# Kernel tuning notes

Hardware: AMD Instinct MI355X
Metric: run time of the kernel (lower is better)

Reference implementation:

```python
import jax, jax.numpy as jnp
import numpy as np

FP8_MAX = 448.0  # float8_e4m3fn max
NUM_HEADS = 16

def _fp8_quant_dequant(t):
    # per-(batch, head) symmetric scaling into fp8 e4m3 range, cast to fp8 and back
    amax = jnp.max(jnp.abs(t), axis=(-2, -1), keepdims=True)
    scale = FP8_MAX / jnp.maximum(amax, 1e-12)
    t8 = (t * scale).astype(jnp.float8_e4m3fn).astype(t.dtype)
    return t8 / scale

def setup_inputs() -> dict:
    key = jax.random.key(0)
    k1, k2, k3 = jax.random.split(key, 3)
    B, N, C = 2, 2048, 1024
    x = jax.random.normal(k1, (B, N, C), dtype=jnp.float32)
    w_qkv = jax.random.normal(k2, (C, 3 * C), dtype=jnp.float32) * (C ** -0.5)
    w_proj = jax.random.normal(k3, (C, C), dtype=jnp.float32) * (C ** -0.5)
    b_proj = jnp.zeros((C,), dtype=jnp.float32)
    return {"x": x, "w_qkv": w_qkv, "w_proj": w_proj, "b_proj": b_proj}

def reference(x, w_qkv, w_proj, b_proj):
    B, N, C = x.shape
    H = NUM_HEADS
    D = C // H
    scale = D ** -0.5
    qkv = (x @ w_qkv).reshape(B, N, 3, H, D).transpose(2, 0, 3, 1, 4)  # [3,B,H,N,D]
    q, k, v = qkv[0], qkv[1], qkv[2]
    # sage-style fp8 quantize/dequant of q and k fused into score computation
    q = _fp8_quant_dequant(q)
    k = _fp8_quant_dequant(k)
    scores = jnp.einsum('bhqd,bhkd->bhqk', q, k) * scale  # [B,H,N,N]
    causal = jnp.tril(jnp.ones((N, N), dtype=bool))
    scores = jnp.where(causal[None, None], scores, jnp.finfo(scores.dtype).min)
    attn = jax.nn.softmax(scores, axis=-1)
    out = jnp.einsum('bhqk,bhkd->bhqd', attn, v)  # [B,H,N,D]
    out = out.transpose(0, 2, 1, 3).reshape(B, N, C)
    return out @ w_proj + b_proj
```

## Files before the change

kernel.cpp:

```cpp
#include <hip/hip_runtime.h>

#define B_   2
#define N_   2048
#define C_   1024
#define H_   16
#define D_   64
#define BH_  (B_*H_)
#define NDH  (N_*D_)
#define M1   (B_*N_)

typedef __attribute__((ext_vector_type(4))) float    f32x4;
typedef __attribute__((ext_vector_type(8))) _Float16 f16x8;
typedef __attribute__((ext_vector_type(4))) _Float16 f16x4;

#define GLOAD_LDS(gp, lp) \
  __builtin_amdgcn_global_load_lds((const __attribute__((address_space(1))) void*)(gp), \
                                   (__attribute__((address_space(3))) void*)(lp), 16, 0, 0)

__global__ void k_cvt16(const float* __restrict__ in, _Float16* __restrict__ out, int n4) {
  int i = blockIdx.x * blockDim.x + threadIdx.x;
  if (i >= n4) return;
  float4 v = ((const float4*)in)[i];
  f16x4 o;
  o.x = (_Float16)v.x; o.y = (_Float16)v.y; o.z = (_Float16)v.z; o.w = (_Float16)v.w;
  ((f16x4*)out)[i] = o;
}

__global__ __launch_bounds__(256) void k_transmerge(const float* __restrict__ wq,
                                                    const float* __restrict__ wp,
                                                    _Float16* __restrict__ whT,
                                                    _Float16* __restrict__ wpT,
                                                    unsigned* __restrict__ amax_u) {
  if (blockIdx.x == 0 && threadIdx.x < 64) amax_u[threadIdx.x] = 0u;
  __shared__ _Float16 t[64][68];
  int idx = blockIdx.x;
  const float* in; _Float16* out; int Cc, cx, cy;
  if (idx < 768) { in = wq; out = whT; Cc = 3072; cx = idx % 48; cy = idx / 48; }
  else { idx -= 768; in = wp; out = wpT; Cc = 1024; cx = idx % 16; cy = idx / 16; }
  const int R = 1024;
  int c0 = cx * 64, r0 = cy * 64;
  int tid = threadIdx.x;
  int cq = tid & 15, rq = tid >> 4;
#pragma unroll
  for (int i = 0; i < 4; ++i) {
    int r = rq + i * 16;
    float4 v = *(const float4*)(in + (size_t)(r0 + r) * Cc + c0 + cq * 4);
    t[r][cq*4+0] = (_Float16)v.x;
    t[r][cq*4+1] = (_Float16)v.y;
    t[r][cq*4+2] = (_Float16)v.z;
    t[r][cq*4+3] = (_Float16)v.w;
  }
  __syncthreads();
#pragma unroll
  for (int i = 0; i < 4; ++i) {
    int c = rq + i * 16;
    f16x4 o;
    o.x = t[cq*4+0][c];
    o.y = t[cq*4+1][c];
    o.z = t[cq*4+2][c];
    o.w = t[cq*4+3][c];
    *(f16x4*)(out + (size_t)(c0 + c) * R + r0 + cq * 4) = o;
  }
}

__global__ __launch_bounds__(256) void k_gemm_qkv(const _Float16* __restrict__ A,
                                                  const _Float16* __restrict__ BT,
                                                  _Float16* __restrict__ qh,
                                                  _Float16* __restrict__ kh,
                                                  _Float16* __restrict__ vh,
                                                  unsigned* __restrict__ amax_u) {
  __shared__ __align__(16) _Float16 As[128 * 32];
  __shared__ __align__(16) _Float16 Bs[128 * 32];
  const int tid = threadIdx.x, lane = tid & 63, wave = tid >> 6;
  const int wm = wave >> 1, wn = wave & 1;
  const int mcol = lane & 15, quad = lane >> 4;
  const int m0 = blockIdx.x * 128, n0 = blockIdx.y * 128;
  f32x4 acc[4][4] = {};
  for (int k0 = 0; k0 < 1024; k0 += 32) {
#pragma unroll
    for (int r = 0; r < 2; ++r) {
      int c = tid + r * 256;
      int row = c >> 2, kc = c & 3;
      GLOAD_LDS(A  + (size_t)(m0 + row) * 1024 + k0 + kc * 8, &As[c * 8]);
      GLOAD_LDS(BT + (size_t)(n0 + row) * 1024 + k0 + kc * 8, &Bs[c * 8]);
    }
    __syncthreads();
    f16x8 af[4], bf[4];
#pragma unroll
    for (int tm = 0; tm < 4; ++tm)
      af[tm] = *(const f16x8*)&As[(wm * 64 + tm * 16 + mcol) * 32 + quad * 8];
#pragma unroll
    for (int tn = 0; tn < 4; ++tn)
      bf[tn] = *(const f16x8*)&Bs[(wn * 64 + tn * 16 + mcol) * 32 + quad * 8];
#pragma unroll
    for (int tm = 0; tm < 4; ++tm)
#pragma unroll
      for (int tn = 0; tn < 4; ++tn)
        acc[tm][tn] = __builtin_amdgcn_mfma_f32_16x16x32_f16(af[tm], bf[tn], acc[tm][tn], 0, 0, 0);
    __syncthreads();
  }
  const int sec = n0 >> 10;
  if (sec < 2) {
    _Float16* dst = sec ? kh : qh;
    float mxv = 0.f;
#pragma unroll
    for (int tm = 0; tm < 4; ++tm)
#pragma unroll
      for (int tn = 0; tn < 4; ++tn) {
        int rowb = m0 + wm * 64 + tm * 16 + quad * 4;
        int col = n0 + wn * 64 + tn * 16 + mcol;
        int cc = col & 1023, h = cc >> 6, d = cc & 63;
        int b = rowb >> 11, n = rowb & 2047;
        f32x4 a = acc[tm][tn];
        mxv = fmaxf(mxv, fmaxf(fmaxf(fabsf(a[0]), fabsf(a[1])),
                               fmaxf(fabsf(a[2]), fabsf(a[3]))));
        f16x4 o;
        o.x = (_Float16)a[0]; o.y = (_Float16)a[1];
        o.z = (_Float16)a[2]; o.w = (_Float16)a[3];
        *(f16x4*)&dst[(size_t)(b * 16 + h) * 131072 + (size_t)(n >> 5) * 2048 + d * 32 + (n & 31)] = o;
      }
#pragma unroll
    for (int off = 32; off; off >>= 1) mxv = fmaxf(mxv, __shfl_xor(mxv, off));
    if (lane == 0) {
      int head = ((n0 & 1023) >> 6) + wn;
      int plane = (m0 >> 11) * 16 + head;
      atomicMax(&amax_u[sec * 32 + plane], __float_as_uint(mxv));
    }
  } else {
#pragma unroll
    for (int tm = 0; tm < 4; ++tm)
#pragma unroll
      for (int tn = 0; tn < 4; ++tn) {
        int rowb = m0 + wm * 64 + tm * 16 + quad * 4;
        int col = n0 + wn * 64 + tn * 16 + mcol;
        int cc = col & 1023, h = cc >> 6, d = cc & 63;
        int b = rowb >> 11, n = rowb & 2047;
        f16x4 o;
        o.x = (_Float16)acc[tm][tn][0];
        o.y = (_Float16)acc[tm][tn][1];
        o.z = (_Float16)acc[tm][tn][2];
        o.w = (_Float16)acc[tm][tn][3];
        *(f16x4*)&vh[(size_t)(b * 16 + h) * 131072 + (size_t)(n >> 5) * 2048 + d * 32 + (n & 31)] = o;
      }
  }
}

__global__ __launch_bounds__(256) void k_quant(const _Float16* __restrict__ qh,
                                               const _Float16* __restrict__ kh,
                                               const float* __restrict__ amax,
                                               char* __restrict__ q8,
                                               char* __restrict__ k8) {
  __shared__ ushort T[32][72];
  int blk = blockIdx.x;
  int which = blk >> 11;
  int idx = blk & 2047;
  int bh = idx >> 6, chunk = idx & 63;
  const _Float16* src = (which ? kh : qh) + (size_t)bh * NDH + chunk * 2048;
  float s = 448.f / fmaxf(amax[which * 32 + bh], 1e-12f);
  int t = threadIdx.x;
  f16x8 v = *(const f16x8*)(src + t * 8);
  int d = t >> 2, kk0 = (t & 3) * 8;
#pragma unroll
  for (int j = 0; j < 8; ++j) T[kk0 + j][d] = ((const ushort*)&v)[j];
  __syncthreads();
  int r = t >> 3, d0 = (t & 7) * 8;
  f16x8 row = *(const f16x8*)&T[r][d0];
  float f[8];
#pragma unroll
  for (int j = 0; j < 8; ++j) f[j] = (float)((const _Float16*)&row)[j] * s;
  int lo = 0, hi = 0;
  lo = __builtin_amdgcn_cvt_pk_fp8_f32(f[0], f[1], lo, false);
  lo = __builtin_amdgcn_cvt_pk_fp8_f32(f[2], f[3], lo, true);
  hi = __builtin_amdgcn_cvt_pk_fp8_f32(f[4], f[5], hi, false);
  hi = __builtin_amdgcn_cvt_pk_fp8_f32(f[6], f[7], hi, true);
  int2 o; o.x = lo; o.y = hi;
  if (which == 0) {
    char* dst = q8 + (size_t)bh * NDH + (size_t)(chunk * 32 + r) * 64 + d0;
    *(int2*)dst = o;
  } else {
    int e = (r >> 2) & 1;
    int mc = (r >> 3) * 4 + (r & 3);
    int kb = d0 >> 5, dq = (d0 >> 3) & 3;
    char* dst = k8 + (size_t)bh * NDH + chunk * 2048 + (e * 2 + kb) * 512 + mc * 32 + dq * 8;
    *(int2*)dst = o;
  }
}

__global__ __launch_bounds__(256, 2) void k_flash(const char* __restrict__ q8,
                                                  const char* __restrict__ k8,
                                                  const _Float16* __restrict__ vh,
                                                  const float* __restrict__ amax,
                                                  _Float16* __restrict__ attn) {
  const int bh = blockIdx.x;
  const int wave = threadIdx.x >> 6, lane = threadIdx.x & 63;
  const int mcol = lane & 15, quad = lane >> 4;
  const int pr = blockIdx.y * 4 + wave;
  const int ga = pr, gb = 127 - pr;
  const int ta = (ga >> 3) + 1;

  float sq = 448.f / fmaxf(amax[bh], 1e-12f);
  float sk = 448.f / fmaxf(amax[32 + bh], 1e-12f);
  const float c2 = (1.f / (sq * sk)) * 0.125f * 1.44269504089f;

  const size_t pbase = (size_t)bh * NDH;
  const char* kbase = k8 + pbase + mcol * 32 + quad * 8;
  const _Float16* vbase = vh + pbase + mcol * 32 + quad * 8;
  const int qrowA = ga * 16 + mcol, qrowB = gb * 16 + mcol;
  long aqA0, aqA1, aqB0, aqB1;
  { const char* qp = q8 + pbase + (size_t)qrowA * 64;
    aqA0 = *(const long*)(qp + quad * 8); aqA1 = *(const long*)(qp + 32 + quad * 8); }
  { const char* qp = q8 + pbase + (size_t)qrowB * 64;
    aqB0 = *(const long*)(qp + quad * 8); aqB1 = *(const long*)(qp + 32 + quad * 8); }

  f32x4 O[4] = {};
  float m_i = -3e38f, l_i = 0.f;
  const int b = bh >> 4, h = bh & 15;
  const int kq = quad * 8;

  long kc[16], kn[16];
  {
    const char* kp = kbase;
#pragma unroll
    for (int i = 0; i < 16; ++i) kc[i] = *(const long*)(kp + i * 512);
  }

  auto body = [&](int t, long (&cur)[16], long (&nxt)[16]) {
    const bool inB = t >= ta;
    const int n0 = (inB ? t - ta : t) * 128;
    const long aq0 = inB ? aqB0 : aqA0;
    const long aq1 = inB ? aqB1 : aqA1;
    const int qrow = inB ? qrowB : qrowA;
    const bool last = inB ? (t == 16) : (t == ta - 1);

    f32x4 s[4][2];
#pragma unroll
    for (int p = 0; p < 4; ++p)
#pragma unroll
      for (int e = 0; e < 2; ++e) {
        f32x4 z = {};
        z = __builtin_amdgcn_mfma_f32_16x16x32_fp8_fp8(cur[p * 4 + e * 2 + 0], aq0, z, 0, 0, 0);
        z = __builtin_amdgcn_mfma_f32_16x16x32_fp8_fp8(cur[p * 4 + e * 2 + 1], aq1, z, 0, 0, 0);
        s[p][e] = z;
      }
    f16x8 va[4][4];
    {
      const _Float16* vp = vbase + (size_t)(n0 >> 5) * 2048;
#pragma unroll
      for (int p = 0; p < 4; ++p)
#pragma unroll
        for (int dt = 0; dt < 4; ++dt)
          va[dt][p] = *(const f16x8*)(vp + p * 2048 + dt * 512);
    }
    if (t < 16) {
      const int t2 = t + 1;
      const int n02 = ((t2 >= ta) ? t2 - ta : t2) * 128;
      const char* kp = kbase + (size_t)(n02 >> 5) * 2048;
#pragma unroll
      for (int i = 0; i < 16; ++i) nxt[i] = *(const long*)(kp + i * 512);
    }
    if (last) {
#pragma unroll
      for (int p = 0; p < 4; ++p)
#pragma unroll
        for (int e = 0; e < 2; ++e)
#pragma unroll
          for (int r = 0; r < 4; ++r) {
            int key = n0 + p * 32 + kq + e * 4 + r;
            float v = s[p][e][r] * c2;
            s[p][e][r] = (key <= qrow) ? v : -3e38f;
          }
    } else {
#pragma unroll
      for (int p = 0; p < 4; ++p)
#pragma unroll
        for (int e = 0; e < 2; ++e)
#pragma unroll
          for (int r = 0; r < 4; ++r)
            s[p][e][r] = s[p][e][r] * c2;
    }
    float fm[8];
#pragma unroll
    for (int p = 0; p < 4; ++p)
#pragma unroll
      for (int e = 0; e < 2; ++e) {
        f32x4 v = s[p][e];
        fm[p * 2 + e] = fmaxf(fmaxf(v[0], v[1]), fmaxf(v[2], v[3]));
      }
    float mx = fmaxf(fmaxf(fmaxf(fm[0], fm[1]), fmaxf(fm[2], fm[3])),
                     fmaxf(fmaxf(fm[4], fm[5]), fmaxf(fm[6], fm[7])));
    mx = fmaxf(mx, m_i);
    mx = fmaxf(mx, __shfl_xor(mx, 16));
    mx = fmaxf(mx, __shfl_xor(mx, 32));
    float alpha = exp2f(m_i - mx);
    m_i = mx;
    float fs[8];
#pragma unroll
    for (int p = 0; p < 4; ++p)
#pragma unroll
      for (int e = 0; e < 2; ++e) {
        float p0 = exp2f(s[p][e][0] - mx);
        float p1 = exp2f(s[p][e][1] - mx);
        float p2 = exp2f(s[p][e][2] - mx);
        float p3 = exp2f(s[p][e][3] - mx);
        s[p][e][0] = p0; s[p][e][1] = p1; s[p][e][2] = p2; s[p][e][3] = p3;
        fs[p * 2 + e] = (p0 + p1) + (p2 + p3);
      }
    float sum = ((fs[0] + fs[1]) + (fs[2] + fs[3])) + ((fs[4] + fs[5]) + (fs[6] + fs[7]));
    sum += __shfl_xor(sum, 16);
    sum += __shfl_xor(sum, 32);
    l_i = l_i * alpha + sum;
#pragma unroll
    for (int dt = 0; dt < 4; ++dt)
#pragma unroll
      for (int r = 0; r < 4; ++r)
        O[dt][r] *= alpha;
#pragma unroll
    for (int p = 0; p < 4; ++p) {
      f16x8 pb;
      pb[0] = (_Float16)s[p][0][0]; pb[1] = (_Float16)s[p][0][1];
      pb[2] = (_Float16)s[p][0][2]; pb[3] = (_Float16)s[p][0][3];
      pb[4] = (_Float16)s[p][1][0]; pb[5] = (_Float16)s[p][1][1];
      pb[6] = (_Float16)s[p][1][2]; pb[7] = (_Float16)s[p][1][3];
#pragma unroll
      for (int dt = 0; dt < 4; ++dt)
        O[dt] = __builtin_amdgcn_mfma_f32_16x16x32_f16(va[dt][p], pb, O[dt], 0, 0, 0);
    }
    if (last) {
      float rl = 1.f / l_i;
      _Float16* op = attn + ((size_t)b * 2048 + qrow) * 1024 + h * 64;
#pragma unroll
      for (int dt = 0; dt < 4; ++dt) {
        f16x4 o;
        o.x = (_Float16)(O[dt][0] * rl);
        o.y = (_Float16)(O[dt][1] * rl);
        o.z = (_Float16)(O[dt][2] * rl);
        o.w = (_Float16)(O[dt][3] * rl);
        *(f16x4*)(op + dt * 16 + quad * 4) = o;
        O[dt] = (f32x4){0.f, 0.f, 0.f, 0.f};
      }
      m_i = -3e38f; l_i = 0.f;
    }
  };

#pragma unroll 1
  for (int t = 0; t < 17; t += 2) {
    body(t, kc, kn);
    if (t + 1 < 17) body(t + 1, kn, kc);
  }
}

__global__ __launch_bounds__(256) void k_gemm_out(const _Float16* __restrict__ A,
                                                  const _Float16* __restrict__ BT,
                                                  const float* __restrict__ bias,
                                                  float* __restrict__ out) {
  __shared__ __align__(16) _Float16 As[128 * 32];
  __shared__ __align__(16) _Float16 Bs[128 * 32];
  const int tid = threadIdx.x, lane = tid & 63, wave = tid >> 6;
  const int wm = wave >> 1, wn = wave & 1;
  const int mcol = lane & 15, quad = lane >> 4;
  const int m0 = blockIdx.x * 128, n0 = blockIdx.y * 128;
  f32x4 acc[4][4] = {};
  for (int k0 = 0; k0 < 1024; k0 += 32) {
#pragma unroll
    for (int r = 0; r < 2; ++r) {
      int c = tid + r * 256;
      int row = c >> 2, kc = c & 3;
      GLOAD_LDS(A  + (size_t)(m0 + row) * 1024 + k0 + kc * 8, &As[c * 8]);
      GLOAD_LDS(BT + (size_t)(n0 + row) * 1024 + k0 + kc * 8, &Bs[c * 8]);
    }
    __syncthreads();
    f16x8 af[4], bf[4];
#pragma unroll
    for (int tm = 0; tm < 4; ++tm)
      af[tm] = *(const f16x8*)&As[(wm * 64 + tm * 16 + mcol) * 32 + quad * 8];
#pragma unroll
    for (int tn = 0; tn < 4; ++tn)
      bf[tn] = *(const f16x8*)&Bs[(wn * 64 + tn * 16 + mcol) * 32 + quad * 8];
#pragma unroll
    for (int tm = 0; tm < 4; ++tm)
#pragma unroll
      for (int tn = 0; tn < 4; ++tn)
        acc[tm][tn] = __builtin_amdgcn_mfma_f32_16x16x32_f16(af[tm], bf[tn], acc[tm][tn], 0, 0, 0);
    __syncthreads();
  }
#pragma unroll
  for (int tm = 0; tm < 4; ++tm)
#pragma unroll
    for (int tn = 0; tn < 4; ++tn)
#pragma unroll
      for (int reg = 0; reg < 4; ++reg) {
        int row = m0 + wm * 64 + tm * 16 + quad * 4 + reg;
        int col = n0 + wn * 64 + tn * 16 + mcol;
        out[(size_t)row * 1024 + col] = acc[tm][tn][reg] + bias[col];
      }
}

extern "C" void kernel_launch(void* const* d_in, const int* in_sizes, int n_in,
                              void* d_out, int out_size, void* d_ws, size_t ws_size,
                              hipStream_t stream) {
  const float* x      = (const float*)d_in[0];
  const float* w_qkv  = (const float*)d_in[1];
  const float* w_proj = (const float*)d_in[2];
  const float* b_proj = (const float*)d_in[3];
  float* out = (float*)d_out;

  char* ws = (char*)d_ws;
  _Float16* xh   = (_Float16*)ws; ws += (size_t)M1 * C_ * 2;
  _Float16* whT  = (_Float16*)ws; ws += (size_t)3 * C_ * C_ * 2;
  _Float16* wpT  = (_Float16*)ws; ws += (size_t)C_ * C_ * 2;
  _Float16* qh   = (_Float16*)ws; ws += (size_t)BH_ * NDH * 2;
  _Float16* kh   = (_Float16*)ws; ws += (size_t)BH_ * NDH * 2;
  _Float16* vh   = (_Float16*)ws; ws += (size_t)BH_ * NDH * 2;
  char*     q8   = (char*)ws;     ws += (size_t)BH_ * NDH;
  char*     k8   = (char*)ws;     ws += (size_t)BH_ * NDH;
  _Float16* attn = (_Float16*)ws; ws += (size_t)M1 * C_ * 2;
  float*    amx  = (float*)ws;    ws += 256;

  k_cvt16<<<(M1 * C_ / 4 + 255) / 256, 256, 0, stream>>>(x, xh, M1 * C_ / 4);
  k_transmerge<<<1024, 256, 0, stream>>>(w_qkv, w_proj, whT, wpT, (unsigned*)amx);
  k_gemm_qkv<<<dim3(M1 / 128, 3 * C_ / 128), 256, 0, stream>>>(xh, whT, qh, kh, vh, (unsigned*)amx);
  k_quant<<<4096, 256, 0, stream>>>(qh, kh, amx, q8, k8);
  k_flash<<<dim3(32, 16), 256, 0, stream>>>(q8, k8, vh, amx, attn);
  k_gemm_out<<<dim3(M1 / 128, C_ / 128), 256, 0, stream>>>(attn, wpT, b_proj, out);
}
```

Before: 216.0 us.

## Split paired causal query tiles into separate waves and fold score scale into exp

Each wave previously handled two paired 16-row query tiles (a short one and a long one) so every wave did an equal 17 key-tile iterations. Now each wave handles a single query tile, ordered longest first, and the grid doubles so more blocks run concurrently; launch bounds go up to 4 blocks per SIMD. The per-element score scaling is folded into the exp2 argument through an fma, and the fp16 packing switches to packed round-toward-zero conversions. This trades the built-in load balance for higher occupancy and a simpler loop, which risks imbalance tails and register pressure under the tighter launch bound.

```diff
diff --git a/kernel.cpp b/kernel.cpp
--- a/kernel.cpp
+++ b/kernel.cpp
@@ -12,6 +12,7 @@
 typedef __attribute__((ext_vector_type(4))) float    f32x4;
 typedef __attribute__((ext_vector_type(8))) _Float16 f16x8;
 typedef __attribute__((ext_vector_type(4))) _Float16 f16x4;
+typedef __attribute__((ext_vector_type(2))) __fp16   h16x2;
 
 #define GLOAD_LDS(gp, lp) \
   __builtin_amdgcn_global_load_lds((const __attribute__((address_space(1))) void*)(gp), \
@@ -186,7 +187,7 @@
   }
 }
 
-__global__ __launch_bounds__(256, 2) void k_flash(const char* __restrict__ q8,
+__global__ __launch_bounds__(256, 4) void k_flash(const char* __restrict__ q8,
                                                   const char* __restrict__ k8,
                                                   const _Float16* __restrict__ vh,
                                                   const float* __restrict__ amax,
@@ -194,9 +195,9 @@
   const int bh = blockIdx.x;
   const int wave = threadIdx.x >> 6, lane = threadIdx.x & 63;
   const int mcol = lane & 15, quad = lane >> 4;
-  const int pr = blockIdx.y * 4 + wave;
-  const int ga = pr, gb = 127 - pr;
-  const int ta = (ga >> 3) + 1;
+  const int slot = blockIdx.y * 4 + wave;
+  const int g = 127 - slot;
+  const int nt = (g >> 3) + 1;
 
   float sq = 448.f / fmaxf(amax[bh], 1e-12f);
   float sk = 448.f / fmaxf(amax[32 + bh], 1e-12f);
@@ -205,12 +206,10 @@
   const size_t pbase = (size_t)bh * NDH;
   const char* kbase = k8 + pbase + mcol * 32 + quad * 8;
   const _Float16* vbase = vh + pbase + mcol * 32 + quad * 8;
-  const int qrowA = ga * 16 + mcol, qrowB = gb * 16 + mcol;
-  long aqA0, aqA1, aqB0, aqB1;
-  { const char* qp = q8 + pbase + (size_t)qrowA * 64;
-    aqA0 = *(const long*)(qp + quad * 8); aqA1 = *(const long*)(qp + 32 + quad * 8); }
-  { const char* qp = q8 + pbase + (size_t)qrowB * 64;
-    aqB0 = *(const long*)(qp + quad * 8); aqB1 = *(const long*)(qp + 32 + quad * 8); }
+  const int qrow = g * 16 + mcol;
+  long aq0, aq1;
+  { const char* qp = q8 + pbase + (size_t)qrow * 64;
+    aq0 = *(const long*)(qp + quad * 8); aq1 = *(const long*)(qp + 32 + quad * 8); }
 
   f32x4 O[4] = {};
   float m_i = -3e38f, l_i = 0.f;
@@ -225,12 +224,8 @@
   }
 
   auto body = [&](int t, long (&cur)[16], long (&nxt)[16]) {
-    const bool inB = t >= ta;
-    const int n0 = (inB ? t - ta : t) * 128;
-    const long aq0 = inB ? aqB0 : aqA0;
-    const long aq1 = inB ? aqB1 : aqA1;
-    const int qrow = inB ? qrowB : qrowA;
-    const bool last = inB ? (t == 16) : (t == ta - 1);
+    const int n0 = t * 128;
+    const bool last = (t == nt - 1);
 
     f32x4 s[4][2];
 #pragma unroll
@@ -251,10 +246,8 @@
         for (int dt = 0; dt < 4; ++dt)
           va[dt][p] = *(const f16x8*)(vp + p * 2048 + dt * 512);
     }
-    if (t < 16) {
-      const int t2 = t + 1;
-      const int n02 = ((t2 >= ta) ? t2 - ta : t2) * 128;
-      const char* kp = kbase + (size_t)(n02 >> 5) * 2048;
+    if (t + 1 < nt) {
+      const char* kp = kbase + (size_t)((n0 + 128) >> 5) * 2048;
 #pragma unroll
       for (int i = 0; i < 16; ++i) nxt[i] = *(const long*)(kp + i * 512);
     }
@@ -266,17 +259,8 @@
 #pragma unroll
           for (int r = 0; r < 4; ++r) {
             int key = n0 + p * 32 + kq + e * 4 + r;
-            float v = s[p][e][r] * c2;
-            s[p][e][r] = (key <= qrow) ? v : -3e38f;
+            s[p][e][r] = (key <= qrow) ? s[p][e][r] : -3e38f;
           }
-    } else {
-#pragma unroll
-      for (int p = 0; p < 4; ++p)
-#pragma unroll
-        for (int e = 0; e < 2; ++e)
-#pragma unroll
-          for (int r = 0; r < 4; ++r)
-            s[p][e][r] = s[p][e][r] * c2;
     }
     float fm[8];
 #pragma unroll
@@ -291,17 +275,18 @@
     mx = fmaxf(mx, m_i);
     mx = fmaxf(mx, __shfl_xor(mx, 16));
     mx = fmaxf(mx, __shfl_xor(mx, 32));
-    float alpha = exp2f(m_i - mx);
+    float alpha = exp2f((m_i - mx) * c2);
     m_i = mx;
+    const float nh = -mx * c2;
     float fs[8];
 #pragma unroll
     for (int p = 0; p < 4; ++p)
 #pragma unroll
       for (int e = 0; e < 2; ++e) {
-        float p0 = exp2f(s[p][e][0] - mx);
-        float p1 = exp2f(s[p][e][1] - mx);
-        float p2 = exp2f(s[p][e][2] - mx);
-        float p3 = exp2f(s[p][e][3] - mx);
+        float p0 = exp2f(fmaf(s[p][e][0], c2, nh));
+        float p1 = exp2f(fmaf(s[p][e][1], c2, nh));
+        float p2 = exp2f(fmaf(s[p][e][2], c2, nh));
+        float p3 = exp2f(fmaf(s[p][e][3], c2, nh));
         s[p][e][0] = p0; s[p][e][1] = p1; s[p][e][2] = p2; s[p][e][3] = p3;
         fs[p * 2 + e] = (p0 + p1) + (p2 + p3);
       }
@@ -317,10 +302,11 @@
 #pragma unroll
     for (int p = 0; p < 4; ++p) {
       f16x8 pb;
-      pb[0] = (_Float16)s[p][0][0]; pb[1] = (_Float16)s[p][0][1];
-      pb[2] = (_Float16)s[p][0][2]; pb[3] = (_Float16)s[p][0][3];
-      pb[4] = (_Float16)s[p][1][0]; pb[5] = (_Float16)s[p][1][1];
-      pb[6] = (_Float16)s[p][1][2]; pb[7] = (_Float16)s[p][1][3];
+      h16x2* pb2 = (h16x2*)&pb;
+      pb2[0] = __builtin_amdgcn_cvt_pkrtz(s[p][0][0], s[p][0][1]);
+      pb2[1] = __builtin_amdgcn_cvt_pkrtz(s[p][0][2], s[p][0][3]);
+      pb2[2] = __builtin_amdgcn_cvt_pkrtz(s[p][1][0], s[p][1][1]);
+      pb2[3] = __builtin_amdgcn_cvt_pkrtz(s[p][1][2], s[p][1][3]);
 #pragma unroll
       for (int dt = 0; dt < 4; ++dt)
         O[dt] = __builtin_amdgcn_mfma_f32_16x16x32_f16(va[dt][p], pb, O[dt], 0, 0, 0);
@@ -336,16 +322,14 @@
         o.z = (_Float16)(O[dt][2] * rl);
         o.w = (_Float16)(O[dt][3] * rl);
         *(f16x4*)(op + dt * 16 + quad * 4) = o;
-        O[dt] = (f32x4){0.f, 0.f, 0.f, 0.f};
-      }
-      m_i = -3e38f; l_i = 0.f;
+      }
     }
   };
 
 #pragma unroll 1
-  for (int t = 0; t < 17; t += 2) {
+  for (int t = 0; t < nt; t += 2) {
     body(t, kc, kn);
-    if (t + 1 < 17) body(t + 1, kn, kc);
+    if (t + 1 < nt) body(t + 1, kn, kc);
   }
 }
 
@@ -420,6 +404,6 @@
   k_transmerge<<<1024, 256, 0, stream>>>(w_qkv, w_proj, whT, wpT, (unsigned*)amx);
   k_gemm_qkv<<<dim3(M1 / 128, 3 * C_ / 128), 256, 0, stream>>>(xh, whT, qh, kh, vh, (unsigned*)amx);
   k_quant<<<4096, 256, 0, stream>>>(qh, kh, amx, q8, k8);
-  k_flash<<<dim3(32, 16), 256, 0, stream>>>(q8, k8, vh, amx, attn);
+  k_flash<<<dim3(32, 32), 256, 0, stream>>>(q8, k8, vh, amx, attn);
   k_gemm_out<<<dim3(M1 / 128, C_ / 128), 256, 0, stream>>>(attn, wpT, b_proj, out);
 }
```

Measured after the change: 350.8 us. +62.4%, slower.
